# Optimization experiments

Measured on AMD Instinct MI355X. Metric: run time of the kernel, lower is better.

## Reference

```python
import jax, jax.numpy as jnp
import numpy as np
from jax import lax

NUM_LAYERS = 4
D_MODEL = 768
D_STATE = 128
D_CONV = 4
EXPAND = 2
HEADDIM = 64
D_INNER = EXPAND * D_MODEL            # 1536
NHEADS = D_INNER // HEADDIM           # 24
NGROUPS = 1
CONV_DIM = D_INNER + 2 * NGROUPS * D_STATE        # 1792 (x, B, C go through conv)
D_PROJ = 2 * D_INNER + 2 * NGROUPS * D_STATE + NHEADS  # z, xBC, dt
BATCH, SEQ = 4, 2048


def silu(x):
    return x * jax.nn.sigmoid(x)


def rmsnorm(x, w, eps):
    xf = x.astype(jnp.float32)
    var = jnp.mean(xf * xf, axis=-1, keepdims=True)
    return (w * (xf * lax.rsqrt(var + eps)).astype(x.dtype))


def ssd_scan(xh, dt, A, B, C):
    # xh: (b,s,h,p)  dt: (b,s,h)  A: (h,)  B,C: (b,s,n)
    b = xh.shape[0]
    dA = jnp.exp(dt * A)  # (b,s,h)
    # time-major for scan
    dA_s = dA.transpose(1, 0, 2)          # (s,b,h)
    dt_s = dt.transpose(1, 0, 2)          # (s,b,h)
    x_s = xh.transpose(1, 0, 2, 3)        # (s,b,h,p)
    B_s = B.transpose(1, 0, 2)            # (s,b,n)
    C_s = C.transpose(1, 0, 2)            # (s,b,n)

    h0 = jnp.zeros((b, NHEADS, HEADDIM, D_STATE), xh.dtype)

    def step(h, inp):
        dA_t, dt_t, x_t, B_t, C_t = inp
        # h_t = exp(dt*A) * h_{t-1} + dt * x outer B
        dBx = (dt_t[:, :, None, None] * x_t[:, :, :, None]) * B_t[:, None, None, :]
        h = dA_t[:, :, None, None] * h + dBx
        y = jnp.einsum('bhpn,bn->bhp', h, C_t)
        return h, y

    _, ys = lax.scan(step, h0, (dA_s, dt_s, x_s, B_s, C_s))
    return ys.transpose(1, 0, 2, 3)  # (b,s,h,p)


def mamba2_block(x, Wi, cw, cb, dtb, Alog, Dp, gw, Wo):
    b, s, _ = x.shape
    zxbcdt = jnp.einsum('bsd,ed->bse', x, Wi)  # (b,s,D_PROJ)
    z = zxbcdt[..., :D_INNER]
    xBC = zxbcdt[..., D_INNER:D_INNER + CONV_DIM]
    dt = zxbcdt[..., D_INNER + CONV_DIM:]

    # causal depthwise conv over time on (x,B,C)
    xc = xBC.transpose(0, 2, 1)  # (b, conv_dim, s)
    xc = lax.conv_general_dilated(xc, cw[:, None, :], (1,), [(D_CONV - 1, 0)],
                                  feature_group_count=CONV_DIM)
    xc = xc + cb[None, :, None]
    xBC = silu(xc.transpose(0, 2, 1))

    x_ssm = xBC[..., :D_INNER]
    Bm = xBC[..., D_INNER:D_INNER + D_STATE]
    Cm = xBC[..., D_INNER + D_STATE:]

    dt = jax.nn.softplus(dt + dtb)           # (b,s,h)
    A = -jnp.exp(Alog)                       # (h,)
    xh = x_ssm.reshape(b, s, NHEADS, HEADDIM)

    y = ssd_scan(xh, dt, A, Bm, Cm) + Dp[None, None, :, None] * xh
    y = y.reshape(b, s, D_INNER)
    y = y * silu(z)                          # gated
    y = rmsnorm(y, gw, 1e-5)
    return jnp.einsum('bse,de->bsd', y, Wo)


def setup_inputs() -> dict:
    key = jax.random.key(0)
    ks = jax.random.split(key, 12)
    L = NUM_LAYERS
    sc_in = 1.0 / np.sqrt(D_MODEL)
    sc_out = 1.0 / np.sqrt(D_INNER)
    sc_conv = np.sqrt(2.0 / D_CONV)
    u = jax.random.uniform(ks[5], (L, NHEADS), minval=1e-3, maxval=0.1)
    return {
        'x': jax.random.normal(ks[0], (BATCH, SEQ, D_MODEL), jnp.float32),
        'in_proj_w': jax.random.normal(ks[1], (L, D_PROJ, D_MODEL), jnp.float32) * sc_in,
        'conv_w': jax.random.normal(ks[2], (L, CONV_DIM, D_CONV), jnp.float32) * sc_conv,
        'conv_b': jnp.zeros((L, CONV_DIM), jnp.float32),
        'dt_bias': jnp.log(jnp.expm1(u)),
        'A_log': jnp.log(jax.random.uniform(ks[6], (L, NHEADS), minval=1.0, maxval=16.0)),
        'D_skip': jnp.ones((L, NHEADS), jnp.float32),
        'gnorm_w': jnp.ones((L, D_INNER), jnp.float32),
        'out_proj_w': jax.random.normal(ks[7], (L, D_MODEL, D_INNER), jnp.float32) * sc_out,
        'ln_w': jnp.ones((L, D_MODEL), jnp.float32),
        'final_ln_w': jnp.ones((D_MODEL,), jnp.float32),
    }


def reference(x, in_proj_w, conv_w, conv_b, dt_bias, A_log, D_skip, gnorm_w,
              out_proj_w, ln_w, final_ln_w):
    for l in range(NUM_LAYERS):
        residual = x
        h = rmsnorm(x, ln_w[l], 1e-6)
        h = mamba2_block(h, in_proj_w[l], conv_w[l], conv_b[l], dt_bias[l],
                         A_log[l], D_skip[l], gnorm_w[l], out_proj_w[l])
        x = h + residual
    return rmsnorm(x, final_ln_w, 1e-6)
```

## Files before the change

kernel.cpp:

```cpp
#include <hip/hip_runtime.h>
#include <hip/hip_bf16.h>
#include <math.h>

#define NUM_LAYERS 4
#define D_MODEL 768
#define D_STATE 128
#define D_CONV 4
#define HEADDIM 64
#define D_INNER 1536
#define NHEADS 24
#define CONV_DIM 1792
#define D_PROJ 3352
#define BATCH 4
#define SEQ 2048
#define NROWS (BATCH*SEQ)
#define CHUNK 128
#define NCHUNK (SEQ/CHUNK)
#define LOG2E 1.4426950408889634f

typedef __bf16 bf16x8 __attribute__((ext_vector_type(8)));
typedef float f32x4 __attribute__((ext_vector_type(4)));

#define GLL(gsrc, ldst)                                                        \
  __builtin_amdgcn_global_load_lds(                                            \
      (const __attribute__((address_space(1))) unsigned int*)(gsrc),           \
      (__attribute__((address_space(3))) unsigned int*)(ldst), 16, 0, 0)

__device__ __forceinline__ float warp_reduce_sum(float v) {
  v += __shfl_xor(v, 32);
  v += __shfl_xor(v, 16);
  v += __shfl_xor(v, 8);
  v += __shfl_xor(v, 4);
  v += __shfl_xor(v, 2);
  v += __shfl_xor(v, 1);
  return v;
}

__device__ __forceinline__ float softplusf(float x) {
  return (x > 20.f) ? x : log1pf(expf(x));
}
__device__ __forceinline__ float siluf(float x) {
  return x / (1.f + expf(-x));
}

__device__ __forceinline__ void store_val(float v, float* p) { *p = v; }
__device__ __forceinline__ void store_val(float v, __hip_bfloat16* p) {
  *p = __float2bfloat16(v);
}

__global__ __launch_bounds__(256) void f32_to_bf16_kernel(
    const float* __restrict__ in, __hip_bfloat16* __restrict__ out, size_t n) {
  for (size_t i = ((size_t)blockIdx.x * 256 + threadIdx.x) * 4; i < n;
       i += (size_t)gridDim.x * 256 * 4) {
    float4 v = *(const float4*)(in + i);
    __hip_bfloat16 h0 = __float2bfloat16(v.x), h1 = __float2bfloat16(v.y);
    __hip_bfloat16 h2 = __float2bfloat16(v.z), h3 = __float2bfloat16(v.w);
    ushort4 u;
    u.x = *(unsigned short*)&h0; u.y = *(unsigned short*)&h1;
    u.z = *(unsigned short*)&h2; u.w = *(unsigned short*)&h3;
    *(ushort4*)(out + i) = u;
  }
}

template <typename OUT>
__global__ __launch_bounds__(256) void rmsnorm768_kernel(
    const float* __restrict__ in, const float* __restrict__ w,
    OUT* __restrict__ out, float eps) {
  int row = blockIdx.x;
  const float* x = in + (size_t)row * D_MODEL;
  OUT* o = out + (size_t)row * D_MODEL;
  int t = threadIdx.x;
  float v0 = x[t], v1 = x[t + 256], v2 = x[t + 512];
  float ss = v0 * v0 + v1 * v1 + v2 * v2;
  __shared__ float sred[4];
  ss = warp_reduce_sum(ss);
  if ((t & 63) == 0) sred[t >> 6] = ss;
  __syncthreads();
  float tot = sred[0] + sred[1] + sred[2] + sred[3];
  float inv = rsqrtf(tot / (float)D_MODEL + eps);
  store_val(w[t] * v0 * inv, o + t);
  store_val(w[t + 256] * v1 * inv, o + t + 256);
  store_val(w[t + 512] * v2 * inv, o + t + 512);
}

#define GEMM_PROLOGUE_AND_MAINLOOP(Asrc, Wsrc, Kdim)                           \
  int t = threadIdx.x;                                                         \
  int w = t >> 6, l = t & 63;                                                  \
  int NT = (Kdim) >> 5;                                                        \
  int ldsA0 = (w * 64) * 8;                                                    \
  int ldsA1 = (256 + w * 64) * 8;                                              \
  int lr = l & 15, lk = l >> 4;                                                \
  int wr = w >> 1, wc = w & 1;                                                 \
  int aoff = (lk * 128 + wr * 64 + lr) * 8;                                    \
  int boff = (lk * 128 + wc * 64 + lr) * 8;                                    \
  f32x4 acc[4][4];                                                             \
  _Pragma("unroll") for (int i = 0; i < 4; i++)                                \
      _Pragma("unroll") for (int j = 0; j < 4; j++) acc[i][j] = (f32x4)0.f;    \
  STAGE(0, 0);                                                                 \
  for (int kt = 0; kt < NT; ++kt) {                                            \
    int cur = kt & 1;                                                          \
    if (kt + 1 < NT) {                                                         \
      STAGE(cur ^ 1, (kt + 1) * 32);                                           \
      asm volatile("s_waitcnt vmcnt(4)" ::: "memory");                         \
    } else {                                                                   \
      asm volatile("s_waitcnt vmcnt(0)" ::: "memory");                         \
    }                                                                          \
    __builtin_amdgcn_sched_barrier(0);                                         \
    __builtin_amdgcn_s_barrier();                                              \
    __builtin_amdgcn_sched_barrier(0);                                         \
    bf16x8 av[4], bv[4];                                                       \
    _Pragma("unroll") for (int mi = 0; mi < 4; mi++)                           \
        av[mi] = *(const bf16x8*)&At[cur][aoff + mi * 128];                    \
    _Pragma("unroll") for (int ni = 0; ni < 4; ni++)                           \
        bv[ni] = *(const bf16x8*)&Bt[cur][boff + ni * 128];                    \
    __builtin_amdgcn_s_setprio(1);                                             \
    _Pragma("unroll") for (int mi = 0; mi < 4; mi++)                           \
        _Pragma("unroll") for (int ni = 0; ni < 4; ni++)                       \
            acc[mi][ni] = __builtin_amdgcn_mfma_f32_16x16x32_bf16(             \
                av[mi], bv[ni], acc[mi][ni], 0, 0, 0);                         \
    __builtin_amdgcn_s_setprio(0);                                             \
    __builtin_amdgcn_sched_barrier(0);                                         \
    __builtin_amdgcn_s_barrier();                                              \
  }

#define STAGE(buf, kofs)                                                       \
  do {                                                                         \
    GLL(Aptr + (kofs), &At[buf][ldsA0]);                                       \
    GLL(Aptr + (kofs) + 16, &At[buf][ldsA1]);                                  \
    GLL(Wptr + (kofs), &Bt[buf][ldsA0]);                                       \
    GLL(Wptr + (kofs) + 16, &Bt[buf][ldsA1]);                                  \
  } while (0)

__global__ __launch_bounds__(256) void gemm_bf16_kernel(
    const __hip_bfloat16* __restrict__ A, const __hip_bfloat16* __restrict__ W,
    const float* __restrict__ res, float* __restrict__ C,
    int M, int N, int K) {
  __shared__ __bf16 At[2][4096];
  __shared__ __bf16 Bt[2][4096];
  int cpx = gridDim.x >> 3;
  int bid = blockIdx.x;
  int bid2 = (bid & 7) * cpx + (bid >> 3);
  int nbn = (N + 127) >> 7;
  int bn = bid2 % nbn;
  int bm = bid2 / nbn;
  int m0 = bm * 128, n0 = bn * 128;
  int srow = threadIdx.x & 127;
  int kbase = (threadIdx.x >> 7) * 8;
  const __hip_bfloat16* Aptr = A + (size_t)(m0 + srow) * K + kbase;
  int nrow = n0 + srow; if (nrow >= N) nrow = N - 1;
  const __hip_bfloat16* Wptr = W + (size_t)nrow * K + kbase;

  GEMM_PROLOGUE_AND_MAINLOOP(A, W, K)

  int rbase = (l >> 4) * 4;
#pragma unroll
  for (int ni = 0; ni < 4; ni++) {
    int n = n0 + wc * 64 + ni * 16 + (l & 15);
    if (n >= N) continue;
#pragma unroll
    for (int mi = 0; mi < 4; mi++) {
#pragma unroll
      for (int r = 0; r < 4; r++) {
        int m = m0 + wr * 64 + mi * 16 + rbase + r;
        float v = acc[mi][ni][r];
        if (res) v += res[(size_t)m * N + n];
        C[(size_t)m * N + n] = v;
      }
    }
  }
}

__global__ __launch_bounds__(512, 1) void gemm_inproj_kernel(
    const __hip_bfloat16* __restrict__ A, const __hip_bfloat16* __restrict__ W,
    __hip_bfloat16* __restrict__ zout, __hip_bfloat16* __restrict__ xout,
    float* __restrict__ dtout) {
  const int K = D_MODEL, N = D_PROJ;
  __shared__ __bf16 ring[3][16384];
  int cpx = gridDim.x >> 3;
  int bid = blockIdx.x;
  int bid2 = (bid & 7) * cpx + (bid >> 3);
  int bn = bid2 % 14;
  int bm = bid2 / 14;
  int m0 = bm * 256, n0 = bn * 256;
  int t = threadIdx.x;
  int w = t >> 6, l = t & 63;
  int lr = l & 15, lk = l >> 4;
  int wr = w >> 2, wc = w & 3;

  const __hip_bfloat16* Aptr[2];
  const __hip_bfloat16* Wptr[2];
  int dOff[2];
#pragma unroll
  for (int i = 0; i < 2; i++) {
    int idx = i * 8 + w;
    int oct = idx >> 2, rb = idx & 3;
    dOff[i] = oct * 2048 + rb * 512;
    Aptr[i] = A + (size_t)(m0 + rb * 64 + l) * K + oct * 8;
    int wrow = n0 + rb * 64 + l; if (wrow >= N) wrow = N - 1;
    Wptr[i] = W + (size_t)wrow * K + oct * 8;
  }

#define STAGE_S(slot, kt)                                                     \
  do {                                                                        \
    _Pragma("unroll") for (int i = 0; i < 2; i++)                             \
        GLL(Aptr[i] + (kt) * 32, &ring[slot][dOff[i]]);                       \
    _Pragma("unroll") for (int i = 0; i < 2; i++)                             \
        GLL(Wptr[i] + (kt) * 32, &ring[slot][8192 + dOff[i]]);                \
  } while (0)

  f32x4 acc[8][4];
#pragma unroll
  for (int i = 0; i < 8; i++)
#pragma unroll
    for (int j = 0; j < 4; j++) acc[i][j] = (f32x4)0.f;

  const int NT = 24;
  STAGE_S(0, 0);
  STAGE_S(1, 1);
  for (int kt = 0; kt < NT; ++kt) {
    int s = kt % 3;
    if (kt + 2 < NT) {
      STAGE_S((kt + 2) % 3, kt + 2);
      asm volatile("s_waitcnt vmcnt(8)" ::: "memory");
    } else if (kt + 1 < NT) {
      asm volatile("s_waitcnt vmcnt(4)" ::: "memory");
    } else {
      asm volatile("s_waitcnt vmcnt(0)" ::: "memory");
    }
    __builtin_amdgcn_sched_barrier(0);
    __builtin_amdgcn_s_barrier();
    __builtin_amdgcn_sched_barrier(0);
    bf16x8 av[8], bv[4];
#pragma unroll
    for (int mi = 0; mi < 8; mi++)
      av[mi] = *(const bf16x8*)&ring[s][lk * 2048 + (wr * 128 + mi * 16 + lr) * 8];
#pragma unroll
    for (int ni = 0; ni < 4; ni++)
      bv[ni] = *(const bf16x8*)&ring[s][8192 + lk * 2048 + (wc * 64 + ni * 16 + lr) * 8];
    __builtin_amdgcn_s_setprio(1);
#pragma unroll
    for (int mi = 0; mi < 8; mi++)
#pragma unroll
      for (int ni = 0; ni < 4; ni++)
        acc[mi][ni] = __builtin_amdgcn_mfma_f32_16x16x32_bf16(
            av[mi], bv[ni], acc[mi][ni], 0, 0, 0);
    __builtin_amdgcn_s_setprio(0);
    __builtin_amdgcn_sched_barrier(0);
    __builtin_amdgcn_s_barrier();
  }
#undef STAGE_S

  int rbase = lk * 4;
  if (bn < 6) {
#pragma unroll
    for (int ni = 0; ni < 4; ni++) {
      int n = n0 + wc * 64 + ni * 16 + lr;
#pragma unroll
      for (int mi = 0; mi < 8; mi++)
#pragma unroll
        for (int r = 0; r < 4; r++) {
          int m = m0 + wr * 128 + mi * 16 + rbase + r;
          zout[(size_t)m * D_INNER + n] = __float2bfloat16(acc[mi][ni][r]);
        }
    }
  } else if (bn < 13) {
    int nb = n0 - D_INNER;
#pragma unroll
    for (int ni = 0; ni < 4; ni++) {
      int n = nb + wc * 64 + ni * 16 + lr;
#pragma unroll
      for (int mi = 0; mi < 8; mi++)
#pragma unroll
        for (int r = 0; r < 4; r++) {
          int m = m0 + wr * 128 + mi * 16 + rbase + r;
          xout[(size_t)m * CONV_DIM + n] = __float2bfloat16(acc[mi][ni][r]);
        }
    }
  } else {
#pragma unroll
    for (int ni = 0; ni < 4; ni++) {
      int loc = wc * 64 + ni * 16 + lr;
      if (loc >= 24) continue;
#pragma unroll
      for (int mi = 0; mi < 8; mi++)
#pragma unroll
        for (int r = 0; r < 4; r++) {
          int m = m0 + wr * 128 + mi * 16 + rbase + r;
          dtout[(size_t)m * 24 + loc] = acc[mi][ni][r];
        }
    }
  }
}

__global__ __launch_bounds__(128) void dt_kernel(
    const float* __restrict__ dtraw, const float* __restrict__ dt_bias,
    const float* __restrict__ A_log, float* __restrict__ dtbuf,
    float* __restrict__ cum2buf) {
  int c = blockIdx.x & 15;
  int h = (blockIdx.x >> 4) % NHEADS;
  int b = blockIdx.x / (16 * NHEADS);
  int t = threadIdx.x;
  int s = c * CHUNK + t;
  float Ah = -expf(A_log[h]);
  float raw = dtraw[((size_t)b * SEQ + s) * 24 + h] + dt_bias[h];
  float dt = softplusf(raw);
  __shared__ float sc[128];
  sc[t] = dt * Ah;
  __syncthreads();
  for (int off = 1; off < 128; off <<= 1) {
    float v = (t >= off) ? sc[t - off] : 0.f;
    __syncthreads();
    sc[t] += v;
    __syncthreads();
  }
  size_t o = ((size_t)b * NHEADS + h) * SEQ + s;
  dtbuf[o] = dt;
  cum2buf[o] = sc[t] * LOG2E;
}

__global__ __launch_bounds__(256) void conv_tiles_kernel(
    const __hip_bfloat16* __restrict__ xbc, const float* __restrict__ cw,
    const float* __restrict__ cb, __hip_bfloat16* __restrict__ xA,
    __hip_bfloat16* __restrict__ Bkt, __hip_bfloat16* __restrict__ Bkn,
    __hip_bfloat16* __restrict__ Ckn) {
  __shared__ float srows[11 * CONV_DIM];
  int to = blockIdx.x & 15;
  int c  = (blockIdx.x >> 4) & 15;
  int b  = blockIdx.x >> 8;
  int t  = threadIdx.x;
  int sb = c * CHUNK + to * 8;
  const __hip_bfloat16* base = xbc + (size_t)b * SEQ * CONV_DIM;
  for (int e = t; e < 11 * 224; e += 256) {
    int r = e / 224, c8 = (e - r * 224) * 8;
    int s = sb - 3 + r;
    float* dst = &srows[r * CONV_DIM + c8];
    if (s >= 0) {
      bf16x8 v = *(const bf16x8*)&base[(size_t)s * CONV_DIM + c8];
#pragma unroll
      for (int j = 0; j < 8; j++) dst[j] = (float)v[j];
    } else {
#pragma unroll
      for (int j = 0; j < 8; j++) dst[j] = 0.f;
    }
  }
  __syncthreads();
  int bc = b * 16 + c;
#pragma unroll
  for (int k7 = 0; k7 < 7; k7++) {
    int ch = t + k7 * 256;
    float w0 = cw[ch * 4], w1 = cw[ch * 4 + 1];
    float w2 = cw[ch * 4 + 2], w3 = cw[ch * 4 + 3];
    float bias = cb[ch];
    float out[8];
#pragma unroll
    for (int j = 0; j < 8; j++) {
      float a = bias;
      a = fmaf(srows[(j + 0) * CONV_DIM + ch], w0, a);
      a = fmaf(srows[(j + 1) * CONV_DIM + ch], w1, a);
      a = fmaf(srows[(j + 2) * CONV_DIM + ch], w2, a);
      a = fmaf(srows[(j + 3) * CONV_DIM + ch], w3, a);
      out[j] = siluf(a);
    }
    if (ch < D_INNER) {
      int h = ch >> 6, p = ch & 63;
      bf16x8 v;
#pragma unroll
      for (int j = 0; j < 8; j++) v[j] = (__bf16)out[j];
      *(bf16x8*)&xA[((((size_t)bc * 24 + h) * 16 + to) * 64 + p) * 8] = v;
    } else if (ch < D_INNER + D_STATE) {
      int n = ch - D_INNER;
      bf16x8 v;
#pragma unroll
      for (int j = 0; j < 8; j++) v[j] = (__bf16)out[j];
      *(bf16x8*)&Bkt[(((size_t)bc * 16 + to) * 128 + n) * 8] = v;
      __hip_bfloat16* dst = Bkn + (size_t)bc * 16384 + ((n >> 3) * 128) * 8 + (n & 7);
#pragma unroll
      for (int j = 0; j < 8; j++)
        dst[(to * 8 + j) * 8] = __float2bfloat16(out[j]);
    } else {
      int n = ch - D_INNER - D_STATE;
      __hip_bfloat16* dst = Ckn + (size_t)bc * 16384 + ((n >> 3) * 128) * 8 + (n & 7);
#pragma unroll
      for (int j = 0; j < 8; j++)
        dst[(to * 8 + j) * 8] = __float2bfloat16(out[j]);
    }
  }
}

__global__ __launch_bounds__(256) void ssd_state_kernel(
    const __hip_bfloat16* __restrict__ xA, const __hip_bfloat16* __restrict__ Bkt,
    const float* __restrict__ dtbuf, const float* __restrict__ cum2buf,
    __hip_bfloat16* __restrict__ states) {
  __shared__ __bf16 sX[8192];
  __shared__ __bf16 sB[16384];
  __shared__ float swdt[128];
  int c = blockIdx.x & 15;
  int h = (blockIdx.x >> 4) % NHEADS;
  int b = blockIdx.x / (16 * NHEADS);
  int t = threadIdx.x;
  int l = t & 63, w = t >> 6;
  const __hip_bfloat16* xsrc = xA + ((size_t)(b * 16 + c) * 24 + h) * 8192;
  const __hip_bfloat16* bsrc = Bkt + (size_t)(b * 16 + c) * 16384;
#pragma unroll
  for (int i = 0; i < 4; i++) GLL(xsrc + (i * 256 + t) * 8, &sX[(i * 256 + t) * 8]);
#pragma unroll
  for (int i = 0; i < 8; i++) GLL(bsrc + (i * 256 + t) * 8, &sB[(i * 256 + t) * 8]);
  {
    size_t dto = ((size_t)b * NHEADS + h) * SEQ + c * CHUNK;
    if (t < 128) {
      float total2 = cum2buf[dto + 127];
      swdt[t] = dtbuf[dto + t] * exp2f(total2 - cum2buf[dto + t]);
    }
  }
  __syncthreads();
#pragma unroll
  for (int i = 0; i < 4; i++) {
    int o = i * 256 + t;
    int to = o >> 6;
    bf16x8 v = *(bf16x8*)&sX[o * 8];
#pragma unroll
    for (int j = 0; j < 8; j++)
      v[j] = (__bf16)((float)v[j] * swdt[to * 8 + j]);
    *(bf16x8*)&sX[o * 8] = v;
  }
  __syncthreads();
  int n0w = w * 32;
  f32x4 acc[4][2];
#pragma unroll
  for (int i = 0; i < 4; i++)
#pragma unroll
    for (int j = 0; j < 2; j++) acc[i][j] = (f32x4)0.f;
#pragma unroll
  for (int kk = 0; kk < 4; kk++) {
    int ko = kk * 4 + (l >> 4);
    bf16x8 av[4], bv[2];
#pragma unroll
    for (int mi = 0; mi < 4; mi++)
      av[mi] = *(const bf16x8*)&sX[(ko * 64 + mi * 16 + (l & 15)) * 8];
#pragma unroll
    for (int ni = 0; ni < 2; ni++)
      bv[ni] = *(const bf16x8*)&sB[(ko * 128 + n0w + ni * 16 + (l & 15)) * 8];
#pragma unroll
    for (int mi = 0; mi < 4; mi++)
#pragma unroll
      for (int ni = 0; ni < 2; ni++)
        acc[mi][ni] = __builtin_amdgcn_mfma_f32_16x16x32_bf16(
            av[mi], bv[ni], acc[mi][ni], 0, 0, 0);
  }
  __hip_bfloat16* dst = states + (((size_t)b * NHEADS + h) * 16 + c) * 8192;
#pragma unroll
  for (int mi = 0; mi < 4; mi++)
#pragma unroll
    for (int ni = 0; ni < 2; ni++) {
      int n = n0w + ni * 16 + (l & 15);
#pragma unroll
      for (int r = 0; r < 4; r++) {
        int p = mi * 16 + (l >> 4) * 4 + r;
        dst[((n >> 3) * 64 + p) * 8 + (n & 7)] = __float2bfloat16(acc[mi][ni][r]);
      }
    }
}

__global__ __launch_bounds__(256) void ssd_chunkscan_kernel(
    __hip_bfloat16* __restrict__ states, const float* __restrict__ cum2buf) {
  int q = blockIdx.x & 3;
  int bh = blockIdx.x >> 2;
  int t = threadIdx.x;
  int o = q * 256 + t;
  __hip_bfloat16* base = states + (size_t)bh * NCHUNK * 8192 + (size_t)o * 8;
  const float* c2 = cum2buf + (size_t)bh * SEQ;
  float hacc[8];
#pragma unroll
  for (int j = 0; j < 8; j++) hacc[j] = 0.f;
  for (int c = 0; c < NCHUNK; c++) {
    float eA = exp2f(c2[c * 128 + 127]);
    __hip_bfloat16* p = base + (size_t)c * 8192;
    bf16x8 v = *(bf16x8*)p;
    bf16x8 wv;
#pragma unroll
    for (int j = 0; j < 8; j++) {
      float tmp = (float)v[j];
      wv[j] = (__bf16)hacc[j];
      hacc[j] = fmaf(eA, hacc[j], tmp);
    }
    *(bf16x8*)p = wv;
  }
}

__global__ __launch_bounds__(256) void ssd_output_kernel(
    const __hip_bfloat16* __restrict__ Ckn, const __hip_bfloat16* __restrict__ Bkn,
    const __hip_bfloat16* __restrict__ xA, const __hip_bfloat16* __restrict__ states,
    const float* __restrict__ dtbuf, const float* __restrict__ cum2buf,
    const float* __restrict__ D_skip, __hip_bfloat16* __restrict__ y) {
  __shared__ __bf16 sC[16384];
  __shared__ __bf16 sBS[16384];
  __shared__ __bf16 sXH[8192];
  int c = blockIdx.x & 15;
  int h = (blockIdx.x >> 4) % NHEADS;
  int b = blockIdx.x / (16 * NHEADS);
  int t = threadIdx.x;
  int l = t & 63, w = t >> 6;
  int bc = b * 16 + c;
  const __hip_bfloat16* csrc = Ckn + (size_t)bc * 16384;
  const __hip_bfloat16* bsrc = Bkn + (size_t)bc * 16384;
  const __hip_bfloat16* xsrc = xA + ((size_t)bc * 24 + h) * 8192;
#pragma unroll
  for (int i = 0; i < 8; i++) GLL(csrc + (i * 256 + t) * 8, &sC[(i * 256 + t) * 8]);
#pragma unroll
  for (int i = 0; i < 8; i++) GLL(bsrc + (i * 256 + t) * 8, &sBS[(i * 256 + t) * 8]);
#pragma unroll
  for (int i = 0; i < 4; i++) GLL(xsrc + (i * 256 + t) * 8, &sXH[(i * 256 + t) * 8]);

  size_t dto = ((size_t)b * NHEADS + h) * SEQ + c * CHUNK;
  float cum2_t[8], cum2_tau[8], dt_tau[8];
#pragma unroll
  for (int fm = 0; fm < 2; fm++)
#pragma unroll
    for (int r = 0; r < 4; r++)
      cum2_t[fm * 4 + r] = cum2buf[dto + w * 32 + fm * 16 + (l >> 4) * 4 + r];
#pragma unroll
  for (int fc = 0; fc < 8; fc++) {
    cum2_tau[fc] = cum2buf[dto + fc * 16 + (l & 15)];
    dt_tau[fc] = dtbuf[dto + fc * 16 + (l & 15)];
  }
  float Dh = D_skip[h];
  __syncthreads();

  f32x4 g[2][8];
#pragma unroll
  for (int i = 0; i < 2; i++)
#pragma unroll
    for (int j = 0; j < 8; j++) g[i][j] = (f32x4)0.f;
#pragma unroll
  for (int kk = 0; kk < 4; kk++) {
    int ko = kk * 4 + (l >> 4);
    bf16x8 a0 = *(const bf16x8*)&sC[(ko * 128 + w * 32 + (l & 15)) * 8];
    bf16x8 a1 = *(const bf16x8*)&sC[(ko * 128 + w * 32 + 16 + (l & 15)) * 8];
#pragma unroll
    for (int fc = 0; fc < 8; fc++) {
      bf16x8 bv = *(const bf16x8*)&sBS[(ko * 128 + fc * 16 + (l & 15)) * 8];
      g[0][fc] = __builtin_amdgcn_mfma_f32_16x16x32_bf16(a0, bv, g[0][fc], 0, 0, 0);
      g[1][fc] = __builtin_amdgcn_mfma_f32_16x16x32_bf16(a1, bv, g[1][fc], 0, 0, 0);
    }
  }
  __syncthreads();

#pragma unroll
  for (int fm = 0; fm < 2; fm++)
#pragma unroll
    for (int fc = 0; fc < 8; fc++) {
      int tau = fc * 16 + (l & 15);
#pragma unroll
      for (int r = 0; r < 4; r++) {
        int tt = w * 32 + fm * 16 + (l >> 4) * 4 + r;
        float v = 0.f;
        if (tt >= tau) {
          v = exp2f(cum2_t[fm * 4 + r] - cum2_tau[fc]) * dt_tau[fc] * g[fm][fc][r];
          if (tt == tau) v += Dh;
        }
        sBS[((tau >> 3) * 128 + tt) * 8 + (tau & 7)] = (__bf16)v;
      }
    }
  f32x4 y1[2][4];
#pragma unroll
  for (int i = 0; i < 2; i++)
#pragma unroll
    for (int j = 0; j < 4; j++) y1[i][j] = (f32x4)0.f;
#pragma unroll
  for (int kk = 0; kk < 4; kk++) {
    int ko = kk * 4 + (l >> 4);
    bf16x8 a0 = *(const bf16x8*)&sBS[(ko * 128 + w * 32 + (l & 15)) * 8];
    bf16x8 a1 = *(const bf16x8*)&sBS[(ko * 128 + w * 32 + 16 + (l & 15)) * 8];
#pragma unroll
    for (int fc = 0; fc < 4; fc++) {
      bf16x8 bv = *(const bf16x8*)&sXH[(ko * 64 + fc * 16 + (l & 15)) * 8];
      y1[0][fc] = __builtin_amdgcn_mfma_f32_16x16x32_bf16(a0, bv, y1[0][fc], 0, 0, 0);
      y1[1][fc] = __builtin_amdgcn_mfma_f32_16x16x32_bf16(a1, bv, y1[1][fc], 0, 0, 0);
    }
  }
  __syncthreads();
  const __hip_bfloat16* hsrc = states + (((size_t)b * NHEADS + h) * 16 + c) * 8192;
#pragma unroll
  for (int i = 0; i < 4; i++) GLL(hsrc + (i * 256 + t) * 8, &sXH[(i * 256 + t) * 8]);
  __syncthreads();

  f32x4 y2[2][4];
#pragma unroll
  for (int i = 0; i < 2; i++)
#pragma unroll
    for (int j = 0; j < 4; j++) y2[i][j] = (f32x4)0.f;
#pragma unroll
  for (int kk = 0; kk < 4; kk++) {
    int ko = kk * 4 + (l >> 4);
    bf16x8 a0 = *(const bf16x8*)&sC[(ko * 128 + w * 32 + (l & 15)) * 8];
    bf16x8 a1 = *(const bf16x8*)&sC[(ko * 128 + w * 32 + 16 + (l & 15)) * 8];
#pragma unroll
    for (int fc = 0; fc < 4; fc++) {
      bf16x8 bv = *(const bf16x8*)&sXH[(ko * 64 + fc * 16 + (l & 15)) * 8];
      y2[0][fc] = __builtin_amdgcn_mfma_f32_16x16x32_bf16(a0, bv, y2[0][fc], 0, 0, 0);
      y2[1][fc] = __builtin_amdgcn_mfma_f32_16x16x32_bf16(a1, bv, y2[1][fc], 0, 0, 0);
    }
  }

  __hip_bfloat16* yr = y + ((size_t)b * SEQ + c * CHUNK) * D_INNER + h * 64;
#pragma unroll
  for (int fm = 0; fm < 2; fm++)
#pragma unroll
    for (int r = 0; r < 4; r++) {
      int tt = w * 32 + fm * 16 + (l >> 4) * 4 + r;
      float sdec = exp2f(cum2_t[fm * 4 + r]);
#pragma unroll
      for (int fc = 0; fc < 4; fc++) {
        int p = fc * 16 + (l & 15);
        yr[(size_t)tt * D_INNER + p] =
            __float2bfloat16(y1[fm][fc][r] + sdec * y2[fm][fc][r]);
      }
    }
}

__global__ __launch_bounds__(192) void gate_norm_kernel(
    __hip_bfloat16* __restrict__ y, const __hip_bfloat16* __restrict__ z,
    const float* __restrict__ gw) {
  int row = blockIdx.x;
  const __hip_bfloat16* zr = z + (size_t)row * D_INNER;
  __hip_bfloat16* yr = y + (size_t)row * D_INNER;
  int t = threadIdx.x;
  bf16x8 yv = *(const bf16x8*)&yr[t * 8];
  bf16x8 zv = *(const bf16x8*)&zr[t * 8];
  float vals[8];
  float ss = 0.f;
#pragma unroll
  for (int j = 0; j < 8; j++) {
    float zf = (float)zv[j];
    float v = (float)yv[j] * siluf(zf);
    vals[j] = v;
    ss += v * v;
  }
  __shared__ float sred[3];
  ss = warp_reduce_sum(ss);
  if ((t & 63) == 0) sred[t >> 6] = ss;
  __syncthreads();
  float tot = sred[0] + sred[1] + sred[2];
  float inv = rsqrtf(tot / (float)D_INNER + 1e-5f);
  bf16x8 o;
#pragma unroll
  for (int j = 0; j < 8; j++)
    o[j] = (__bf16)(gw[t * 8 + j] * vals[j] * inv);
  *(bf16x8*)&yr[t * 8] = o;
}

extern "C" void kernel_launch(void* const* d_in, const int* in_sizes, int n_in,
                              void* d_out, int out_size, void* d_ws, size_t ws_size,
                              hipStream_t stream) {
  const float* x          = (const float*)d_in[0];
  const float* in_proj_w  = (const float*)d_in[1];
  const float* conv_w     = (const float*)d_in[2];
  const float* conv_b     = (const float*)d_in[3];
  const float* dt_bias    = (const float*)d_in[4];
  const float* A_log      = (const float*)d_in[5];
  const float* D_skip     = (const float*)d_in[6];
  const float* gnorm_w    = (const float*)d_in[7];
  const float* out_proj_w = (const float*)d_in[8];
  const float* ln_w       = (const float*)d_in[9];
  const float* final_ln_w = (const float*)d_in[10];

  float* ws = (float*)d_ws;
  float* curx   = ws; ws += (size_t)NROWS * D_MODEL;
  float* dtraw  = ws; ws += (size_t)NROWS * 24;
  float* dtbuf  = ws; ws += (size_t)BATCH * NHEADS * SEQ;
  float* cum2   = ws; ws += (size_t)BATCH * NHEADS * SEQ;
  __hip_bfloat16* zbuf   = (__hip_bfloat16*)ws; ws += (size_t)NROWS * D_INNER / 2;
  __hip_bfloat16* xbcbuf = (__hip_bfloat16*)ws; ws += (size_t)NROWS * CONV_DIM / 2;
  __hip_bfloat16* hbuf_b = (__hip_bfloat16*)ws; ws += (size_t)NROWS * D_MODEL / 2;
  __hip_bfloat16* ybuf_b = (__hip_bfloat16*)ws; ws += (size_t)NROWS * D_INNER / 2;
  __hip_bfloat16* wi_b   = (__hip_bfloat16*)ws; ws += (size_t)NUM_LAYERS * D_PROJ * D_MODEL / 2;
  __hip_bfloat16* wo_b   = (__hip_bfloat16*)ws; ws += (size_t)NUM_LAYERS * D_MODEL * D_INNER / 2;
  __hip_bfloat16* xAb    = (__hip_bfloat16*)ws; ws += (size_t)BATCH * NCHUNK * 24 * 8192 / 2;
  __hip_bfloat16* Bkt    = (__hip_bfloat16*)ws; ws += (size_t)BATCH * NCHUNK * 16384 / 2;
  __hip_bfloat16* Bkn    = (__hip_bfloat16*)ws; ws += (size_t)BATCH * NCHUNK * 16384 / 2;
  __hip_bfloat16* Ckn    = (__hip_bfloat16*)ws; ws += (size_t)BATCH * NCHUNK * 16384 / 2;
  __hip_bfloat16* states = (__hip_bfloat16*)ws;

  f32_to_bf16_kernel<<<1024, 256, 0, stream>>>(
      in_proj_w, wi_b, (size_t)NUM_LAYERS * D_PROJ * D_MODEL);
  f32_to_bf16_kernel<<<1024, 256, 0, stream>>>(
      out_proj_w, wo_b, (size_t)NUM_LAYERS * D_MODEL * D_INNER);

  for (int l = 0; l < NUM_LAYERS; l++) {
    const float* xin = (l == 0) ? x : curx;
    rmsnorm768_kernel<__hip_bfloat16><<<NROWS, 256, 0, stream>>>(
        xin, ln_w + (size_t)l * D_MODEL, hbuf_b, 1e-6f);

    gemm_inproj_kernel<<<448, 512, 0, stream>>>(
        hbuf_b, wi_b + (size_t)l * D_PROJ * D_MODEL, zbuf, xbcbuf, dtraw);

    dt_kernel<<<BATCH * NHEADS * NCHUNK, 128, 0, stream>>>(
        dtraw, dt_bias + l * NHEADS, A_log + l * NHEADS, dtbuf, cum2);

    conv_tiles_kernel<<<BATCH * NCHUNK * 16, 256, 0, stream>>>(
        xbcbuf, conv_w + (size_t)l * CONV_DIM * D_CONV,
        conv_b + (size_t)l * CONV_DIM, xAb, Bkt, Bkn, Ckn);

    ssd_state_kernel<<<BATCH * NHEADS * NCHUNK, 256, 0, stream>>>(
        xAb, Bkt, dtbuf, cum2, states);

    ssd_chunkscan_kernel<<<BATCH * NHEADS * 4, 256, 0, stream>>>(states, cum2);

    ssd_output_kernel<<<BATCH * NHEADS * NCHUNK, 256, 0, stream>>>(
        Ckn, Bkn, xAb, states, dtbuf, cum2, D_skip + l * NHEADS, ybuf_b);

    gate_norm_kernel<<<NROWS, 192, 0, stream>>>(
        ybuf_b, zbuf, gnorm_w + (size_t)l * D_INNER);

    gemm_bf16_kernel<<<64 * 6, 256, 0, stream>>>(
        ybuf_b, wo_b + (size_t)l * D_MODEL * D_INNER, xin, curx,
        NROWS, D_MODEL, D_INNER);
  }
  rmsnorm768_kernel<float><<<NROWS, 256, 0, stream>>>(
      curx, final_ln_w, (float*)d_out, 1e-6f);
}
```

Baseline: 1.047 ms.

## Interleave prefetch loads with MFMA phases in in_proj GEMM main loop

Splits each k-step of the in_proj GEMM into eight phases, each followed by a workgroup barrier. The global-to-LDS prefetches for step kt+2 are spread across the first four phases instead of issued in one burst, and the LDS fragment reads are spread across phases alongside groups of four MFMAs. The B fragments are reused in a snake order for the second half of the A rows. The aim is to overlap memory traffic with matrix math and reduce register pressure, at the cost of many more barriers per iteration.

```diff
diff --git a/kernel.cpp b/kernel.cpp
--- a/kernel.cpp
+++ b/kernel.cpp
@@ -200,13 +200,20 @@
     Wptr[i] = W + (size_t)wrow * K + oct * 8;
   }
 
-#define STAGE_S(slot, kt)                                                     \
+#define PH_END()                                                              \
   do {                                                                        \
-    _Pragma("unroll") for (int i = 0; i < 2; i++)                             \
-        GLL(Aptr[i] + (kt) * 32, &ring[slot][dOff[i]]);                       \
-    _Pragma("unroll") for (int i = 0; i < 2; i++)                             \
-        GLL(Wptr[i] + (kt) * 32, &ring[slot][8192 + dOff[i]]);                \
+    __builtin_amdgcn_sched_barrier(0);                                        \
+    __builtin_amdgcn_s_barrier();                                             \
+    __builtin_amdgcn_sched_barrier(0);                                        \
   } while (0)
+#define MFMA4(ACCROW, BV)                                                     \
+  do {                                                                        \
+    __builtin_amdgcn_s_setprio(1);                                            \
+    _Pragma("unroll") for (int mi = 0; mi < 4; mi++)                          \
+        acc[(ACCROW) + mi][ci] = __builtin_amdgcn_mfma_f32_16x16x32_bf16(     \
+            ((ACCROW) ? av1 : av0)[mi], (BV), acc[(ACCROW) + mi][ci], 0, 0, 0);\
+    __builtin_amdgcn_s_setprio(0);                                            \
+  } while (0)
 
   f32x4 acc[8][4];
 #pragma unroll
@@ -215,40 +222,65 @@
     for (int j = 0; j < 4; j++) acc[i][j] = (f32x4)0.f;
 
   const int NT = 24;
-  STAGE_S(0, 0);
-  STAGE_S(1, 1);
+#pragma unroll
+  for (int i = 0; i < 2; i++) {
+    GLL(Aptr[i], &ring[0][dOff[i]]);
+    GLL(Wptr[i], &ring[0][8192 + dOff[i]]);
+  }
+#pragma unroll
+  for (int i = 0; i < 2; i++) {
+    GLL(Aptr[i] + 32, &ring[1][dOff[i]]);
+    GLL(Wptr[i] + 32, &ring[1][8192 + dOff[i]]);
+  }
+
   for (int kt = 0; kt < NT; ++kt) {
     int s = kt % 3;
-    if (kt + 2 < NT) {
-      STAGE_S((kt + 2) % 3, kt + 2);
-      asm volatile("s_waitcnt vmcnt(8)" ::: "memory");
-    } else if (kt + 1 < NT) {
+    int sn = (kt + 2) % 3;
+    bool pf = (kt + 2) < NT;
+    if (kt + 1 < NT) {
       asm volatile("s_waitcnt vmcnt(4)" ::: "memory");
     } else {
       asm volatile("s_waitcnt vmcnt(0)" ::: "memory");
     }
-    __builtin_amdgcn_sched_barrier(0);
-    __builtin_amdgcn_s_barrier();
-    __builtin_amdgcn_sched_barrier(0);
-    bf16x8 av[8], bv[4];
-#pragma unroll
-    for (int mi = 0; mi < 8; mi++)
-      av[mi] = *(const bf16x8*)&ring[s][lk * 2048 + (wr * 128 + mi * 16 + lr) * 8];
-#pragma unroll
-    for (int ni = 0; ni < 4; ni++)
-      bv[ni] = *(const bf16x8*)&ring[s][8192 + lk * 2048 + (wc * 64 + ni * 16 + lr) * 8];
-    __builtin_amdgcn_s_setprio(1);
-#pragma unroll
-    for (int mi = 0; mi < 8; mi++)
-#pragma unroll
-      for (int ni = 0; ni < 4; ni++)
-        acc[mi][ni] = __builtin_amdgcn_mfma_f32_16x16x32_bf16(
-            av[mi], bv[ni], acc[mi][ni], 0, 0, 0);
-    __builtin_amdgcn_s_setprio(0);
-    __builtin_amdgcn_sched_barrier(0);
-    __builtin_amdgcn_s_barrier();
-  }
-#undef STAGE_S
+    PH_END();
+
+    const __bf16* Ab = &ring[s][0];
+    const __bf16* Bb = &ring[s][8192];
+    bf16x8 av0[4], av1[4], bv0, bv1, bv2, bv3;
+    int ci;
+    if (pf) GLL(Aptr[0] + (kt + 2) * 32, &ring[sn][dOff[0]]);
+#pragma unroll
+    for (int mi = 0; mi < 4; mi++)
+      av0[mi] = *(const bf16x8*)&Ab[lk * 2048 + (wr * 128 + mi * 16 + lr) * 8];
+    bv0 = *(const bf16x8*)&Bb[lk * 2048 + (wc * 64 + 0 * 16 + lr) * 8];
+    ci = 0; MFMA4(0, bv0);
+    PH_END();
+    if (pf) GLL(Aptr[1] + (kt + 2) * 32, &ring[sn][dOff[1]]);
+    bv1 = *(const bf16x8*)&Bb[lk * 2048 + (wc * 64 + 1 * 16 + lr) * 8];
+    ci = 1; MFMA4(0, bv1);
+    PH_END();
+    if (pf) GLL(Wptr[0] + (kt + 2) * 32, &ring[sn][8192 + dOff[0]]);
+    bv2 = *(const bf16x8*)&Bb[lk * 2048 + (wc * 64 + 2 * 16 + lr) * 8];
+    ci = 2; MFMA4(0, bv2);
+    PH_END();
+    if (pf) GLL(Wptr[1] + (kt + 2) * 32, &ring[sn][8192 + dOff[1]]);
+    bv3 = *(const bf16x8*)&Bb[lk * 2048 + (wc * 64 + 3 * 16 + lr) * 8];
+    ci = 3; MFMA4(0, bv3);
+    PH_END();
+#pragma unroll
+    for (int mi = 0; mi < 4; mi++)
+      av1[mi] = *(const bf16x8*)&Ab[lk * 2048 + (wr * 128 + (mi + 4) * 16 + lr) * 8];
+    ci = 3; MFMA4(4, bv3);
+    PH_END();
+    ci = 2; MFMA4(4, bv2);
+    PH_END();
+    ci = 1; MFMA4(4, bv1);
+    PH_END();
+    ci = 0; MFMA4(4, bv0);
+    PH_END();
+  }
+#undef PH_END
+#undef MFMA4
 
   int rbase = lk * 4;
   if (bn < 6) {
```

New measurement: 1.009 ms. 1.04x faster.
